# Optimization experiments

Measured on AMD Instinct MI355X. Metric: run time of the kernel, lower is better.

Reference implementation:

```python
import jax, jax.numpy as jnp
import numpy as np

N_NODES = 100000
N_EDGES = 3200000


def setup_inputs() -> dict:
    key = jax.random.key(0)
    k1, k2, k3, k4 = jax.random.split(key, 4)
    x = jax.random.normal(k1, (N_NODES, 3), dtype=jnp.float32)
    edge_index = jax.random.randint(k2, (2, N_EDGES), 0, N_NODES, dtype=jnp.int64)
    # Glorot-ish init for the two GCN layers
    W1 = jax.random.normal(k3, (3, 16), dtype=jnp.float32) * (1.0 / np.sqrt(3.0))
    b1 = jnp.zeros((16,), dtype=jnp.float32)
    W2 = jax.random.normal(k4, (16, 2), dtype=jnp.float32) * (1.0 / np.sqrt(16.0))
    b2 = jnp.zeros((2,), dtype=jnp.float32)
    return {"x": x, "edge_index": edge_index, "W1": W1, "b1": b1, "W2": W2, "b2": b2}


def gcn_conv(x, row, col, W, b, n_nodes):
    """PyG GCNConv: add self-loops, symmetric deg^-1/2 norm, linear, scatter-add, bias.
    row/col already include self-loops."""
    deg = jax.ops.segment_sum(jnp.ones_like(col, dtype=x.dtype), col, num_segments=n_nodes)
    dinv = jnp.where(deg > 0, deg ** -0.5, 0.0)
    norm = dinv[row] * dinv[col]            # [E+N]
    h = x @ W                               # [N, out]
    msg = h[row] * norm[:, None]            # gather + edge scale
    out = jax.ops.segment_sum(msg, col, num_segments=n_nodes)  # scatter-add to targets
    return out + b


def reference(x, edge_index, W1, b1, W2, b2):
    n = x.shape[0]
    loop = jnp.arange(n, dtype=edge_index.dtype)
    row = jnp.concatenate([edge_index[0], loop])
    col = jnp.concatenate([edge_index[1], loop])
    h = jax.nn.relu(gcn_conv(x, row, col, W1, b1, n))
    # dropout is identity in eval mode (training=False)
    h = gcn_conv(h, row, col, W2, b2, n)
    return jax.nn.log_softmax(h, axis=1)
```

## Files before the change

### kernel.cpp

```cpp
#include <hip/hip_runtime.h>
#include <math.h>

#define NN 100000
#define NB 32
#define NRANGE 8
#define RSZ 12500
#define CHUNK 1024
#define NCHUNK 98

#define W_FLAG  0
#define W_CNT   256
#define W_OFF   400256
#define W_DINV  800256
#define W_CSUM  1200256
#define W_CBASE 1201280
#define W_XS    1202304
#define W_HS2   2802304
#define W_B16   3602304
#define W_Z     10002304
#define SZ_RADIX 22802304
#define B_CNT   256
#define B_OFF   400256
#define B_CUR   800256
#define B_DINV  1200256
#define B_CSUM  1600256
#define B_CBASE 1601280
#define B_XS    1602560
#define B_HS2   3202560
#define B_RIDX  4002560
#define SZ_B    16802560

__global__ void k_detect(const void* ei, int* flag) {
    if (blockIdx.x == 0 && threadIdx.x == 0) {
        const long long* p = (const long long*)ei;
        int ok = 1;
        for (int i = 0; i < 64; ++i) {
            long long v = p[i];
            if (v < 0 || v >= NN) { ok = 0; break; }
        }
        *flag = ok;
    }
}

template <typename T>
__device__ __forceinline__ void phist_body(const T* __restrict__ col, long long E,
                                           unsigned* __restrict__ lcnt,
                                           unsigned short* __restrict__ cntP) {
    int r = blockIdx.x & (NRANGE - 1);
    int b = blockIdx.x >> 3;
    unsigned lo = (unsigned)r * RSZ;
    for (int i = threadIdx.x; i < RSZ; i += blockDim.x) lcnt[i] = 0u;
    __syncthreads();
    long long S = (E + NB - 1) / NB;
    long long sb = (long long)b * S;
    long long se = sb + S < E ? sb + S : E;
    long long B = blockDim.x;
    long long base = sb + threadIdx.x;
    long long nfull = (se - sb) / (4 * B);
    for (long long t = 0; t < nfull; ++t) {
        unsigned c0 = (unsigned)col[base];
        unsigned c1 = (unsigned)col[base + B];
        unsigned c2 = (unsigned)col[base + 2 * B];
        unsigned c3 = (unsigned)col[base + 3 * B];
        unsigned d0 = c0 - lo, d1 = c1 - lo, d2 = c2 - lo, d3 = c3 - lo;
        if (d0 < RSZ) atomicAdd(&lcnt[d0], 1u);
        if (d1 < RSZ) atomicAdd(&lcnt[d1], 1u);
        if (d2 < RSZ) atomicAdd(&lcnt[d2], 1u);
        if (d3 < RSZ) atomicAdd(&lcnt[d3], 1u);
        base += 4 * B;
    }
    for (long long e = base; e < se; e += B) {
        unsigned d = (unsigned)col[e] - lo;
        if (d < RSZ) atomicAdd(&lcnt[d], 1u);
    }
    __syncthreads();
    unsigned short* dst = cntP + (size_t)b * NN + lo;
    for (int i = threadIdx.x; i < RSZ; i += blockDim.x) dst[i] = (unsigned short)lcnt[i];
}
__global__ void k_phist(const void* ei, long long E, const int* flag,
                        unsigned short* cntP) {
    __shared__ unsigned lcnt[RSZ];
    if (*flag) phist_body(((const long long*)ei) + E, E, lcnt, cntP);
    else       phist_body(((const int*)ei) + E, E, lcnt, cntP);
}

__global__ void k_scanA(const unsigned short* __restrict__ cntP, unsigned* __restrict__ cnt,
                        unsigned* __restrict__ off, unsigned* __restrict__ csum) {
    __shared__ unsigned lds[256];
    int t = threadIdx.x;
    int base = blockIdx.x * CHUNK + t * 4;
    unsigned v[4] = {0u, 0u, 0u, 0u};
    if (base + 3 < NN) {
#pragma unroll
        for (int b = 0; b < NB; ++b) {
            const unsigned short* p = cntP + (size_t)b * NN + base;
            v[0] += p[0]; v[1] += p[1]; v[2] += p[2]; v[3] += p[3];
        }
    } else {
#pragma unroll
        for (int k = 0; k < 4; ++k) {
            int i = base + k;
            if (i < NN) { unsigned s = 0; for (int b = 0; b < NB; ++b) s += cntP[(size_t)b * NN + i]; v[k] = s; }
        }
    }
#pragma unroll
    for (int k = 0; k < 4; ++k) { int i = base + k; if (i < NN) cnt[i] = v[k]; }
    unsigned s = v[0] + v[1] + v[2] + v[3];
    lds[t] = s; __syncthreads();
    for (int o = 1; o < 256; o <<= 1) {
        unsigned add = (t >= o) ? lds[t - o] : 0u; __syncthreads();
        lds[t] += add; __syncthreads();
    }
    unsigned excl = lds[t] - s;
    if (t == 255) csum[blockIdx.x] = lds[255];
#pragma unroll
    for (int k = 0; k < 4; ++k) { int i = base + k; if (i < NN) off[i] = excl; excl += v[k]; }
}

__global__ void k_scan1(const unsigned* __restrict__ cnt, unsigned* __restrict__ off,
                        unsigned* __restrict__ csum) {
    __shared__ unsigned lds[256];
    int t = threadIdx.x;
    int base = blockIdx.x * CHUNK + t * 4;
    unsigned v[4];
#pragma unroll
    for (int k = 0; k < 4; ++k) { int i = base + k; v[k] = (i < NN) ? cnt[i] : 0u; }
    unsigned s = v[0] + v[1] + v[2] + v[3];
    lds[t] = s; __syncthreads();
    for (int o = 1; o < 256; o <<= 1) {
        unsigned add = (t >= o) ? lds[t - o] : 0u; __syncthreads();
        lds[t] += add; __syncthreads();
    }
    unsigned excl = lds[t] - s;
    if (t == 255) csum[blockIdx.x] = lds[255];
#pragma unroll
    for (int k = 0; k < 4; ++k) { int i = base + k; if (i < NN) off[i] = excl; excl += v[k]; }
}
__global__ void k_scan2(unsigned* __restrict__ csum, unsigned* __restrict__ cbase) {
    __shared__ unsigned lds[256];
    int t = threadIdx.x;
    unsigned s = (t < NCHUNK) ? csum[t] : 0u;
    lds[t] = s; __syncthreads();
    for (int o = 1; o < 256; o <<= 1) {
        unsigned add = (t >= o) ? lds[t - o] : 0u; __syncthreads();
        lds[t] += add; __syncthreads();
    }
    if (t < NCHUNK) cbase[t] = lds[t] - s;
}

__global__ void k_final(const unsigned short* __restrict__ cntP,
                        const unsigned* __restrict__ cbase, const unsigned* __restrict__ cnt,
                        unsigned* __restrict__ off, unsigned short* __restrict__ base16,
                        const float* __restrict__ x, float* __restrict__ dinv,
                        float4* __restrict__ xs) {
    int n = blockIdx.x * blockDim.x + threadIdx.x;
    if (n >= NN) return;
    unsigned o = off[n] + cbase[n >> 10];
    off[n] = o;
    unsigned run = 0;
#pragma unroll
    for (int b = 0; b < NB; ++b) {
        base16[(size_t)b * NN + n] = (unsigned short)run;
        run += cntP[(size_t)b * NN + n];
    }
    float d = rsqrtf((float)cnt[n] + 1.0f);
    dinv[n] = d;
    xs[n] = make_float4(x[3*n] * d, x[3*n+1] * d, x[3*n+2] * d, 0.f);
}

template <typename T>
__device__ __forceinline__ void pplace_body(const T* __restrict__ ei, long long E,
                                            const unsigned* __restrict__ off,
                                            const unsigned short* __restrict__ base16,
                                            unsigned* __restrict__ lcur,
                                            unsigned* __restrict__ ridx) {
    int r = blockIdx.x & (NRANGE - 1);
    int b = blockIdx.x >> 3;
    unsigned lo = (unsigned)r * RSZ;
    const unsigned short* bb = base16 + (size_t)b * NN + lo;
    const unsigned* oo = off + lo;
    for (int i = threadIdx.x; i < RSZ; i += blockDim.x) lcur[i] = oo[i] + bb[i];
    __syncthreads();
    const T* col = ei + E;
    long long S = (E + NB - 1) / NB;
    long long sb = (long long)b * S;
    long long se = sb + S < E ? sb + S : E;
    long long B = blockDim.x;
    long long base = sb + threadIdx.x;
    long long nfull = (se - sb) / (4 * B);
    for (long long t = 0; t < nfull; ++t) {
        long long e0 = base, e1 = base + B, e2 = base + 2 * B, e3 = base + 3 * B;
        unsigned d0 = (unsigned)col[e0] - lo;
        unsigned d1 = (unsigned)col[e1] - lo;
        unsigned d2 = (unsigned)col[e2] - lo;
        unsigned d3 = (unsigned)col[e3] - lo;
        if (d0 < RSZ) { unsigned p = atomicAdd(&lcur[d0], 1u); ridx[p] = (unsigned)ei[e0]; }
        if (d1 < RSZ) { unsigned p = atomicAdd(&lcur[d1], 1u); ridx[p] = (unsigned)ei[e1]; }
        if (d2 < RSZ) { unsigned p = atomicAdd(&lcur[d2], 1u); ridx[p] = (unsigned)ei[e2]; }
        if (d3 < RSZ) { unsigned p = atomicAdd(&lcur[d3], 1u); ridx[p] = (unsigned)ei[e3]; }
        base += 4 * B;
    }
    for (long long e = base; e < se; e += B) {
        unsigned d = (unsigned)col[e] - lo;
        if (d < RSZ) { unsigned p = atomicAdd(&lcur[d], 1u); ridx[p] = (unsigned)ei[e]; }
    }
}
__global__ void k_pplace(const void* ei, long long E, const int* flag,
                         const unsigned* off, const unsigned short* base16,
                         unsigned* ridx) {
    __shared__ unsigned lcur[RSZ];
    if (*flag) pplace_body((const long long*)ei, E, off, base16, lcur, ridx);
    else       pplace_body((const int*)ei, E, off, base16, lcur, ridx);
}

__global__ void k_lay1(const unsigned* __restrict__ off, const unsigned* __restrict__ cnt,
                       const unsigned* __restrict__ ridx, const float4* __restrict__ xs,
                       const float* __restrict__ dinv,
                       const float* __restrict__ W1, const float* __restrict__ b1,
                       const float* __restrict__ W2, float2* __restrict__ hs2) {
    int lane = threadIdx.x & 15;
    int node = blockIdx.x * (blockDim.x >> 4) + (threadIdx.x >> 4);
    if (node >= NN) return;
    unsigned s = off[node], n = cnt[node];
    float a0 = 0.f, a1 = 0.f, a2 = 0.f;
    for (unsigned k = lane; k < n; k += 16) {
        float4 v = xs[ridx[s + k]];
        a0 += v.x; a1 += v.y; a2 += v.z;
    }
#pragma unroll
    for (int m = 8; m; m >>= 1) {
        a0 += __shfl_xor(a0, m); a1 += __shfl_xor(a1, m); a2 += __shfl_xor(a2, m);
    }
    if (lane == 0) {
        float4 sv = xs[node];
        float d = dinv[node];
        float t0 = d*(a0+sv.x), t1 = d*(a1+sv.y), t2 = d*(a2+sv.z);
        float g0 = 0.f, g1 = 0.f;
#pragma unroll
        for (int j = 0; j < 16; ++j) {
            float h = fmaxf(fmaf(t0, W1[j], fmaf(t1, W1[16+j], fmaf(t2, W1[32+j], b1[j]))), 0.f);
            g0 = fmaf(h, W2[2*j],   g0);
            g1 = fmaf(h, W2[2*j+1], g1);
        }
        hs2[node] = make_float2(g0 * d, g1 * d);
    }
}
__global__ void k_lay2(const unsigned* __restrict__ off, const unsigned* __restrict__ cnt,
                       const unsigned* __restrict__ ridx, const float2* __restrict__ hs2,
                       const float* __restrict__ dinv, const float* __restrict__ b2,
                       float2* __restrict__ out) {
    int lane = threadIdx.x & 15;
    int node = blockIdx.x * (blockDim.x >> 4) + (threadIdx.x >> 4);
    if (node >= NN) return;
    unsigned s = off[node], n = cnt[node];
    float a0 = 0.f, a1 = 0.f;
    for (unsigned k = lane; k < n; k += 16) {
        float2 v = hs2[ridx[s + k]];
        a0 += v.x; a1 += v.y;
    }
#pragma unroll
    for (int m = 8; m; m >>= 1) {
        a0 += __shfl_xor(a0, m); a1 += __shfl_xor(a1, m);
    }
    if (lane == 0) {
        float2 sv = hs2[node];
        float d = dinv[node];
        float z0 = d*(a0+sv.x) + b2[0];
        float z1 = d*(a1+sv.y) + b2[1];
        float mx = fmaxf(z0, z1);
        float l  = mx + logf(expf(z0 - mx) + expf(z1 - mx));
        out[node] = make_float2(z0 - l, z1 - l);
    }
}

__global__ void k_zero(float4* z, long long n4) {
    long long stride = (long long)gridDim.x * blockDim.x;
    for (long long i = (long long)blockIdx.x * blockDim.x + threadIdx.x; i < n4; i += stride)
        z[i] = make_float4(0.f, 0.f, 0.f, 0.f);
}
template <typename T>
__device__ __forceinline__ void hist_loop(const T* __restrict__ col, long long E,
                                          unsigned* __restrict__ cnt) {
    long long stride = (long long)gridDim.x * blockDim.x;
    for (long long e = (long long)blockIdx.x * blockDim.x + threadIdx.x; e < E; e += stride)
        atomicAdd(&cnt[(unsigned)col[e]], 1u);
}
__global__ void k_histM(const void* ei, long long E, const int* flag, unsigned* cnt) {
    if (*flag) hist_loop(((const long long*)ei) + E, E, cnt);
    else       hist_loop(((const int*)ei) + E, E, cnt);
}
__global__ void k_scan3(const unsigned* __restrict__ cnt, const unsigned* __restrict__ cbase,
                        unsigned* __restrict__ off, unsigned* __restrict__ cur,
                        const float* __restrict__ x, float* __restrict__ dinv,
                        float4* __restrict__ xs) {
    int i = blockIdx.x * blockDim.x + threadIdx.x;
    if (i >= NN) return;
    unsigned o = off[i] + cbase[i >> 10];
    off[i] = o; cur[i] = o;
    float d = rsqrtf((float)cnt[i] + 1.0f);
    dinv[i] = d;
    xs[i] = make_float4(x[3*i] * d, x[3*i+1] * d, x[3*i+2] * d, 0.f);
}
template <typename T>
__device__ __forceinline__ void placeM_loop(const T* __restrict__ ei, long long E,
                                            unsigned* __restrict__ cur, unsigned* __restrict__ ridx) {
    long long stride = (long long)gridDim.x * blockDim.x;
    for (long long e = (long long)blockIdx.x * blockDim.x + threadIdx.x; e < E; e += stride) {
        unsigned c = (unsigned)ei[E + e];
        unsigned pos = atomicAdd(&cur[c], 1u);
        ridx[pos] = (unsigned)ei[e];
    }
}
__global__ void k_placeM(const void* ei, long long E, const int* flag,
                         unsigned* cur, unsigned* ridx) {
    if (*flag) placeM_loop((const long long*)ei, E, cur, ridx);
    else       placeM_loop((const int*)ei, E, cur, ridx);
}

extern "C" void kernel_launch(void* const* d_in, const int* in_sizes, int n_in,
                              void* d_out, int out_size, void* d_ws, size_t ws_size,
                              hipStream_t stream) {
    const float* x  = (const float*)d_in[0];
    const void*  ei = d_in[1];
    const float* W1 = (const float*)d_in[2];
    const float* b1 = (const float*)d_in[3];
    const float* W2 = (const float*)d_in[4];
    const float* b2 = (const float*)d_in[5];
    long long E = (long long)in_sizes[1] / 2;

    char* ws = (char*)d_ws;
    int* flag = (int*)(ws + W_FLAG);
    float2* out = (float2*)d_out;

    int ngrid = (NN + 255) / 256;
    int lgrid = (NN + 15) / 16;

    k_detect<<<1, 64, 0, stream>>>(ei, flag);

    if (ws_size >= SZ_RADIX) {
        unsigned*       cnt    = (unsigned*)(ws + W_CNT);
        unsigned*       off    = (unsigned*)(ws + W_OFF);
        float*          dinv   = (float*)(ws + W_DINV);
        unsigned*       csum   = (unsigned*)(ws + W_CSUM);
        unsigned*       cbase  = (unsigned*)(ws + W_CBASE);
        float4*         xs     = (float4*)(ws + W_XS);
        float2*         hs2    = (float2*)(ws + W_HS2);
        unsigned short* base16 = (unsigned short*)(ws + W_B16);
        unsigned short* cntP   = (unsigned short*)(ws + W_Z);
        unsigned*       ridx   = (unsigned*)(ws + W_Z);

        k_phist <<<NRANGE * NB, 1024, 0, stream>>>(ei, E, flag, cntP);
        k_scanA <<<NCHUNK, 256, 0, stream>>>(cntP, cnt, off, csum);
        k_scan2 <<<1, 256, 0, stream>>>(csum, cbase);
        k_final <<<ngrid, 256, 0, stream>>>(cntP, cbase, cnt, off, base16, x, dinv, xs);
        k_pplace<<<NRANGE * NB, 1024, 0, stream>>>(ei, E, flag, off, base16, ridx);
        k_lay1  <<<lgrid, 256, 0, stream>>>(off, cnt, ridx, xs, dinv, W1, b1, W2, hs2);
        k_lay2  <<<lgrid, 256, 0, stream>>>(off, cnt, ridx, hs2, dinv, b2, out);
    } else if (ws_size >= SZ_B) {
        unsigned* cnt   = (unsigned*)(ws + B_CNT);
        unsigned* off   = (unsigned*)(ws + B_OFF);
        unsigned* cur   = (unsigned*)(ws + B_CUR);
        float*    dinv  = (float*)(ws + B_DINV);
        unsigned* csum  = (unsigned*)(ws + B_CSUM);
        unsigned* cbase = (unsigned*)(ws + B_CBASE);
        float4*   xs    = (float4*)(ws + B_XS);
        float2*   hs2   = (float2*)(ws + B_HS2);
        unsigned* ridx  = (unsigned*)(ws + B_RIDX);
        long long eg = (E + 255) / 256;
        int egrid = (int)(eg > 4096 ? 4096 : eg);

        k_zero  <<<98, 256, 0, stream>>>((float4*)(ws + B_CNT), 25000);
        k_histM <<<egrid, 256, 0, stream>>>(ei, E, flag, cnt);
        k_scan1 <<<NCHUNK, 256, 0, stream>>>(cnt, off, csum);
        k_scan2 <<<1, 256, 0, stream>>>(csum, cbase);
        k_scan3 <<<ngrid, 256, 0, stream>>>(cnt, cbase, off, cur, x, dinv, xs);
        k_placeM<<<egrid, 256, 0, stream>>>(ei, E, flag, cur, ridx);
        k_lay1  <<<lgrid, 256, 0, stream>>>(off, cnt, ridx, xs, dinv, W1, b1, W2, hs2);
        k_lay2  <<<lgrid, 256, 0, stream>>>(off, cnt, ridx, hs2, dinv, b2, out);
    }
}
```

Measured before the change: 208.7 us.

## Add two-pass bucketed staging of edges before per-range histogram and placement

Result: faster. 176.4 us (-15.5%).

```diff
diff --git a/kernel.cpp b/kernel.cpp
--- a/kernel.cpp
+++ b/kernel.cpp
@@ -5,9 +5,26 @@
 #define NB 32
 #define NRANGE 8
 #define RSZ 12500
+#define NS 256
 #define CHUNK 1024
 #define NCHUNK 98
 
+#define S_FLAG  0
+#define S_BCNT  256
+#define S_BOFF  8448
+#define S_ROFF  16640
+#define S_CNT   16896
+#define S_OFF   416896
+#define S_DINV  816896
+#define S_CSUM  1216896
+#define S_CBASE 1217536
+#define S_XS    1218048
+#define S_HS2   2818048
+#define S_B16   3618048
+#define S_STG   10018048
+#define S_CNTP  22818048
+#define S_RIDX  22818048
+#define SZ_S    35618048
 #define W_FLAG  0
 #define W_CNT   256
 #define W_OFF   400256
@@ -43,45 +60,148 @@
 }
 
 template <typename T>
-__device__ __forceinline__ void phist_body(const T* __restrict__ col, long long E,
-                                           unsigned* __restrict__ lcnt,
-                                           unsigned short* __restrict__ cntP) {
-    int r = blockIdx.x & (NRANGE - 1);
-    int b = blockIdx.x >> 3;
-    unsigned lo = (unsigned)r * RSZ;
-    for (int i = threadIdx.x; i < RSZ; i += blockDim.x) lcnt[i] = 0u;
-    __syncthreads();
-    long long S = (E + NB - 1) / NB;
-    long long sb = (long long)b * S;
-    long long se = sb + S < E ? sb + S : E;
+__device__ __forceinline__ void bcount_body(const T* __restrict__ col, long long E,
+                                            unsigned* __restrict__ lds8,
+                                            unsigned* __restrict__ bucketCnt) {
+    int s = blockIdx.x;
+    for (int i = threadIdx.x; i < 8 * 64; i += blockDim.x) lds8[i] = 0u;
+    __syncthreads();
+    long long S = (E + NS - 1) / NS;
+    long long sb = (long long)s * S, se = sb + S < E ? sb + S : E;
     long long B = blockDim.x;
     long long base = sb + threadIdx.x;
+    int lane = threadIdx.x & 63;
     long long nfull = (se - sb) / (4 * B);
     for (long long t = 0; t < nfull; ++t) {
         unsigned c0 = (unsigned)col[base];
         unsigned c1 = (unsigned)col[base + B];
         unsigned c2 = (unsigned)col[base + 2 * B];
         unsigned c3 = (unsigned)col[base + 3 * B];
-        unsigned d0 = c0 - lo, d1 = c1 - lo, d2 = c2 - lo, d3 = c3 - lo;
-        if (d0 < RSZ) atomicAdd(&lcnt[d0], 1u);
-        if (d1 < RSZ) atomicAdd(&lcnt[d1], 1u);
-        if (d2 < RSZ) atomicAdd(&lcnt[d2], 1u);
-        if (d3 < RSZ) atomicAdd(&lcnt[d3], 1u);
+        atomicAdd(&lds8[(c0 / RSZ) * 64 + lane], 1u);
+        atomicAdd(&lds8[(c1 / RSZ) * 64 + lane], 1u);
+        atomicAdd(&lds8[(c2 / RSZ) * 64 + lane], 1u);
+        atomicAdd(&lds8[(c3 / RSZ) * 64 + lane], 1u);
         base += 4 * B;
     }
+    for (long long e = base; e < se; e += B)
+        atomicAdd(&lds8[((unsigned)col[e] / RSZ) * 64 + lane], 1u);
+    __syncthreads();
+    if (threadIdx.x < 8) {
+        unsigned t = 0;
+        for (int j = 0; j < 64; ++j) t += lds8[threadIdx.x * 64 + j];
+        bucketCnt[s * 8 + threadIdx.x] = t;
+    }
+}
+__global__ void k_bcount(const void* ei, long long E, const int* flag,
+                         unsigned* bucketCnt) {
+    __shared__ unsigned lds8[8 * 64];
+    if (*flag) bcount_body(((const long long*)ei) + E, E, lds8, bucketCnt);
+    else       bcount_body(((const int*)ei) + E, E, lds8, bucketCnt);
+}
+
+__global__ void k_bscan(const unsigned* __restrict__ bucketCnt,
+                        unsigned* __restrict__ bucketOff, unsigned* __restrict__ rangeOff) {
+    __shared__ unsigned lds[1024];
+    int t = threadIdx.x;
+    int j0 = 2 * t, j1 = 2 * t + 1;
+    unsigned v0 = bucketCnt[(j0 & (NS - 1)) * 8 + (j0 >> 8)];
+    unsigned v1 = bucketCnt[(j1 & (NS - 1)) * 8 + (j1 >> 8)];
+    unsigned s = v0 + v1;
+    lds[t] = s; __syncthreads();
+    for (int o = 1; o < 1024; o <<= 1) {
+        unsigned add = (t >= o) ? lds[t - o] : 0u; __syncthreads();
+        lds[t] += add; __syncthreads();
+    }
+    unsigned excl = lds[t] - s;
+    bucketOff[j0] = excl;
+    bucketOff[j1] = excl + v0;
+    if ((j0 & (NS - 1)) == 0) rangeOff[j0 >> 8] = excl;
+    if (t == 1023) rangeOff[8] = lds[1023];
+}
+
+template <typename T>
+__device__ __forceinline__ void stage_body(const T* __restrict__ ei, long long E,
+                                           const unsigned* __restrict__ bucketOff,
+                                           unsigned* __restrict__ lcur,
+                                           unsigned* __restrict__ staged) {
+    int s = blockIdx.x;
+    if (threadIdx.x < 8) lcur[threadIdx.x] = bucketOff[threadIdx.x * NS + s];
+    __syncthreads();
+    const T* col = ei + E;
+    long long S = (E + NS - 1) / NS;
+    long long sb = (long long)s * S, se = sb + S < E ? sb + S : E;
+    long long B = blockDim.x;
+    long long base = sb + threadIdx.x;
+    long long nfull = (se - sb) / (4 * B);
+    for (long long t = 0; t < nfull; ++t) {
+        long long e0 = base, e1 = base + B, e2 = base + 2 * B, e3 = base + 3 * B;
+        unsigned c0 = (unsigned)col[e0], c1 = (unsigned)col[e1];
+        unsigned c2 = (unsigned)col[e2], c3 = (unsigned)col[e3];
+        unsigned r0 = (unsigned)ei[e0], r1 = (unsigned)ei[e1];
+        unsigned r2 = (unsigned)ei[e2], r3 = (unsigned)ei[e3];
+        unsigned g0 = c0 / RSZ, g1 = c1 / RSZ, g2 = c2 / RSZ, g3 = c3 / RSZ;
+        unsigned p0 = atomicAdd(&lcur[g0], 1u);
+        unsigned p1 = atomicAdd(&lcur[g1], 1u);
+        unsigned p2 = atomicAdd(&lcur[g2], 1u);
+        unsigned p3 = atomicAdd(&lcur[g3], 1u);
+        staged[p0] = (r0 << 14) | (c0 - g0 * RSZ);
+        staged[p1] = (r1 << 14) | (c1 - g1 * RSZ);
+        staged[p2] = (r2 << 14) | (c2 - g2 * RSZ);
+        staged[p3] = (r3 << 14) | (c3 - g3 * RSZ);
+        base += 4 * B;
+    }
     for (long long e = base; e < se; e += B) {
-        unsigned d = (unsigned)col[e] - lo;
-        if (d < RSZ) atomicAdd(&lcnt[d], 1u);
-    }
-    __syncthreads();
-    unsigned short* dst = cntP + (size_t)b * NN + lo;
+        unsigned c = (unsigned)col[e], r = (unsigned)ei[e];
+        unsigned g = c / RSZ;
+        unsigned p = atomicAdd(&lcur[g], 1u);
+        staged[p] = (r << 14) | (c - g * RSZ);
+    }
+}
+__global__ void k_stage(const void* ei, long long E, const int* flag,
+                        const unsigned* bucketOff, unsigned* staged) {
+    __shared__ unsigned lcur[8];
+    if (*flag) stage_body((const long long*)ei, E, bucketOff, lcur, staged);
+    else       stage_body((const int*)ei, E, bucketOff, lcur, staged);
+}
+
+__global__ void k_shist(const unsigned* __restrict__ staged, const unsigned* __restrict__ rangeOff,
+                        unsigned short* __restrict__ cntP) {
+    __shared__ unsigned lcnt[RSZ];
+    int r = blockIdx.x & (NRANGE - 1);
+    int s = blockIdx.x >> 3;
+    for (int i = threadIdx.x; i < RSZ; i += blockDim.x) lcnt[i] = 0u;
+    __syncthreads();
+    unsigned A = rangeOff[r], Bnd = rangeOff[r + 1];
+    unsigned L = (Bnd - A + NB - 1) / NB;
+    unsigned cb = A + s * L;
+    unsigned ce = cb + L < Bnd ? cb + L : Bnd;
+    for (unsigned i = cb + threadIdx.x; i < ce; i += blockDim.x)
+        atomicAdd(&lcnt[staged[i] & 16383u], 1u);
+    __syncthreads();
+    unsigned short* dst = cntP + (size_t)s * NN + (unsigned)r * RSZ;
     for (int i = threadIdx.x; i < RSZ; i += blockDim.x) dst[i] = (unsigned short)lcnt[i];
 }
-__global__ void k_phist(const void* ei, long long E, const int* flag,
-                        unsigned short* cntP) {
-    __shared__ unsigned lcnt[RSZ];
-    if (*flag) phist_body(((const long long*)ei) + E, E, lcnt, cntP);
-    else       phist_body(((const int*)ei) + E, E, lcnt, cntP);
+
+__global__ void k_splace(const unsigned* __restrict__ staged, const unsigned* __restrict__ rangeOff,
+                         const unsigned* __restrict__ off, const unsigned short* __restrict__ base16,
+                         unsigned* __restrict__ ridx) {
+    __shared__ unsigned lcur[RSZ];
+    int r = blockIdx.x & (NRANGE - 1);
+    int s = blockIdx.x >> 3;
+    unsigned lo = (unsigned)r * RSZ;
+    const unsigned short* bb = base16 + (size_t)s * NN + lo;
+    const unsigned* oo = off + lo;
+    for (int i = threadIdx.x; i < RSZ; i += blockDim.x) lcur[i] = oo[i] + bb[i];
+    __syncthreads();
+    unsigned A = rangeOff[r], Bnd = rangeOff[r + 1];
+    unsigned L = (Bnd - A + NB - 1) / NB;
+    unsigned cb = A + s * L;
+    unsigned ce = cb + L < Bnd ? cb + L : Bnd;
+    for (unsigned i = cb + threadIdx.x; i < ce; i += blockDim.x) {
+        unsigned p = staged[i];
+        unsigned pos = atomicAdd(&lcur[p & 16383u], 1u);
+        ridx[pos] = p >> 14;
+    }
 }
 
 __global__ void k_scanA(const unsigned short* __restrict__ cntP, unsigned* __restrict__ cnt,
@@ -116,7 +236,6 @@
 #pragma unroll
     for (int k = 0; k < 4; ++k) { int i = base + k; if (i < NN) off[i] = excl; excl += v[k]; }
 }
-
 __global__ void k_scan1(const unsigned* __restrict__ cnt, unsigned* __restrict__ off,
                         unsigned* __restrict__ csum) {
     __shared__ unsigned lds[256];
@@ -147,7 +266,6 @@
     }
     if (t < NCHUNK) cbase[t] = lds[t] - s;
 }
-
 __global__ void k_final(const unsigned short* __restrict__ cntP,
                         const unsigned* __restrict__ cbase, const unsigned* __restrict__ cnt,
                         unsigned* __restrict__ off, unsigned short* __restrict__ base16,
@@ -167,7 +285,105 @@
     dinv[n] = d;
     xs[n] = make_float4(x[3*n] * d, x[3*n+1] * d, x[3*n+2] * d, 0.f);
 }
-
+__global__ void k_lay1(const unsigned* __restrict__ off, const unsigned* __restrict__ cnt,
+                       const unsigned* __restrict__ ridx, const float4* __restrict__ xs,
+                       const float* __restrict__ dinv,
+                       const float* __restrict__ W1, const float* __restrict__ b1,
+                       const float* __restrict__ W2, float2* __restrict__ hs2) {
+    int lane = threadIdx.x & 15;
+    int node = blockIdx.x * (blockDim.x >> 4) + (threadIdx.x >> 4);
+    if (node >= NN) return;
+    unsigned s = off[node], n = cnt[node];
+    float a0 = 0.f, a1 = 0.f, a2 = 0.f;
+    for (unsigned k = lane; k < n; k += 16) {
+        float4 v = xs[ridx[s + k]];
+        a0 += v.x; a1 += v.y; a2 += v.z;
+    }
+#pragma unroll
+    for (int m = 8; m; m >>= 1) {
+        a0 += __shfl_xor(a0, m); a1 += __shfl_xor(a1, m); a2 += __shfl_xor(a2, m);
+    }
+    if (lane == 0) {
+        float4 sv = xs[node];
+        float d = dinv[node];
+        float t0 = d*(a0+sv.x), t1 = d*(a1+sv.y), t2 = d*(a2+sv.z);
+        float g0 = 0.f, g1 = 0.f;
+#pragma unroll
+        for (int j = 0; j < 16; ++j) {
+            float h = fmaxf(fmaf(t0, W1[j], fmaf(t1, W1[16+j], fmaf(t2, W1[32+j], b1[j]))), 0.f);
+            g0 = fmaf(h, W2[2*j],   g0);
+            g1 = fmaf(h, W2[2*j+1], g1);
+        }
+        hs2[node] = make_float2(g0 * d, g1 * d);
+    }
+}
+__global__ void k_lay2(const unsigned* __restrict__ off, const unsigned* __restrict__ cnt,
+                       const unsigned* __restrict__ ridx, const float2* __restrict__ hs2,
+                       const float* __restrict__ dinv, const float* __restrict__ b2,
+                       float2* __restrict__ out) {
+    int lane = threadIdx.x & 15;
+    int node = blockIdx.x * (blockDim.x >> 4) + (threadIdx.x >> 4);
+    if (node >= NN) return;
+    unsigned s = off[node], n = cnt[node];
+    float a0 = 0.f, a1 = 0.f;
+    for (unsigned k = lane; k < n; k += 16) {
+        float2 v = hs2[ridx[s + k]];
+        a0 += v.x; a1 += v.y;
+    }
+#pragma unroll
+    for (int m = 8; m; m >>= 1) {
+        a0 += __shfl_xor(a0, m); a1 += __shfl_xor(a1, m);
+    }
+    if (lane == 0) {
+        float2 sv = hs2[node];
+        float d = dinv[node];
+        float z0 = d*(a0+sv.x) + b2[0];
+        float z1 = d*(a1+sv.y) + b2[1];
+        float mx = fmaxf(z0, z1);
+        float l  = mx + logf(expf(z0 - mx) + expf(z1 - mx));
+        out[node] = make_float2(z0 - l, z1 - l);
+    }
+}
+
+template <typename T>
+__device__ __forceinline__ void phist_body(const T* __restrict__ col, long long E,
+                                           unsigned* __restrict__ lcnt,
+                                           unsigned short* __restrict__ cntP) {
+    int r = blockIdx.x & (NRANGE - 1);
+    int b = blockIdx.x >> 3;
+    unsigned lo = (unsigned)r * RSZ;
+    for (int i = threadIdx.x; i < RSZ; i += blockDim.x) lcnt[i] = 0u;
+    __syncthreads();
+    long long S = (E + NB - 1) / NB;
+    long long sb = (long long)b * S, se = sb + S < E ? sb + S : E;
+    long long B = blockDim.x;
+    long long base = sb + threadIdx.x;
+    long long nfull = (se - sb) / (4 * B);
+    for (long long t = 0; t < nfull; ++t) {
+        unsigned d0 = (unsigned)col[base] - lo;
+        unsigned d1 = (unsigned)col[base + B] - lo;
+        unsigned d2 = (unsigned)col[base + 2 * B] - lo;
+        unsigned d3 = (unsigned)col[base + 3 * B] - lo;
+        if (d0 < RSZ) atomicAdd(&lcnt[d0], 1u);
+        if (d1 < RSZ) atomicAdd(&lcnt[d1], 1u);
+        if (d2 < RSZ) atomicAdd(&lcnt[d2], 1u);
+        if (d3 < RSZ) atomicAdd(&lcnt[d3], 1u);
+        base += 4 * B;
+    }
+    for (long long e = base; e < se; e += B) {
+        unsigned d = (unsigned)col[e] - lo;
+        if (d < RSZ) atomicAdd(&lcnt[d], 1u);
+    }
+    __syncthreads();
+    unsigned short* dst = cntP + (size_t)b * NN + lo;
+    for (int i = threadIdx.x; i < RSZ; i += blockDim.x) dst[i] = (unsigned short)lcnt[i];
+}
+__global__ void k_phist(const void* ei, long long E, const int* flag,
+                        unsigned short* cntP) {
+    __shared__ unsigned lcnt[RSZ];
+    if (*flag) phist_body(((const long long*)ei) + E, E, lcnt, cntP);
+    else       phist_body(((const int*)ei) + E, E, lcnt, cntP);
+}
 template <typename T>
 __device__ __forceinline__ void pplace_body(const T* __restrict__ ei, long long E,
                                             const unsigned* __restrict__ off,
@@ -183,8 +399,7 @@
     __syncthreads();
     const T* col = ei + E;
     long long S = (E + NB - 1) / NB;
-    long long sb = (long long)b * S;
-    long long se = sb + S < E ? sb + S : E;
+    long long sb = (long long)b * S, se = sb + S < E ? sb + S : E;
     long long B = blockDim.x;
     long long base = sb + threadIdx.x;
     long long nfull = (se - sb) / (4 * B);
@@ -213,66 +428,6 @@
     else       pplace_body((const int*)ei, E, off, base16, lcur, ridx);
 }
 
-__global__ void k_lay1(const unsigned* __restrict__ off, const unsigned* __restrict__ cnt,
-                       const unsigned* __restrict__ ridx, const float4* __restrict__ xs,
-                       const float* __restrict__ dinv,
-                       const float* __restrict__ W1, const float* __restrict__ b1,
-                       const float* __restrict__ W2, float2* __restrict__ hs2) {
-    int lane = threadIdx.x & 15;
-    int node = blockIdx.x * (blockDim.x >> 4) + (threadIdx.x >> 4);
-    if (node >= NN) return;
-    unsigned s = off[node], n = cnt[node];
-    float a0 = 0.f, a1 = 0.f, a2 = 0.f;
-    for (unsigned k = lane; k < n; k += 16) {
-        float4 v = xs[ridx[s + k]];
-        a0 += v.x; a1 += v.y; a2 += v.z;
-    }
-#pragma unroll
-    for (int m = 8; m; m >>= 1) {
-        a0 += __shfl_xor(a0, m); a1 += __shfl_xor(a1, m); a2 += __shfl_xor(a2, m);
-    }
-    if (lane == 0) {
-        float4 sv = xs[node];
-        float d = dinv[node];
-        float t0 = d*(a0+sv.x), t1 = d*(a1+sv.y), t2 = d*(a2+sv.z);
-        float g0 = 0.f, g1 = 0.f;
-#pragma unroll
-        for (int j = 0; j < 16; ++j) {
-            float h = fmaxf(fmaf(t0, W1[j], fmaf(t1, W1[16+j], fmaf(t2, W1[32+j], b1[j]))), 0.f);
-            g0 = fmaf(h, W2[2*j],   g0);
-            g1 = fmaf(h, W2[2*j+1], g1);
-        }
-        hs2[node] = make_float2(g0 * d, g1 * d);
-    }
-}
-__global__ void k_lay2(const unsigned* __restrict__ off, const unsigned* __restrict__ cnt,
-                       const unsigned* __restrict__ ridx, const float2* __restrict__ hs2,
-                       const float* __restrict__ dinv, const float* __restrict__ b2,
-                       float2* __restrict__ out) {
-    int lane = threadIdx.x & 15;
-    int node = blockIdx.x * (blockDim.x >> 4) + (threadIdx.x >> 4);
-    if (node >= NN) return;
-    unsigned s = off[node], n = cnt[node];
-    float a0 = 0.f, a1 = 0.f;
-    for (unsigned k = lane; k < n; k += 16) {
-        float2 v = hs2[ridx[s + k]];
-        a0 += v.x; a1 += v.y;
-    }
-#pragma unroll
-    for (int m = 8; m; m >>= 1) {
-        a0 += __shfl_xor(a0, m); a1 += __shfl_xor(a1, m);
-    }
-    if (lane == 0) {
-        float2 sv = hs2[node];
-        float d = dinv[node];
-        float z0 = d*(a0+sv.x) + b2[0];
-        float z1 = d*(a1+sv.y) + b2[1];
-        float mx = fmaxf(z0, z1);
-        float l  = mx + logf(expf(z0 - mx) + expf(z1 - mx));
-        out[node] = make_float2(z0 - l, z1 - l);
-    }
-}
-
 __global__ void k_zero(float4* z, long long n4) {
     long long stride = (long long)gridDim.x * blockDim.x;
     for (long long i = (long long)blockIdx.x * blockDim.x + threadIdx.x; i < n4; i += stride)
@@ -329,15 +484,41 @@
     long long E = (long long)in_sizes[1] / 2;
 
     char* ws = (char*)d_ws;
-    int* flag = (int*)(ws + W_FLAG);
     float2* out = (float2*)d_out;
-
     int ngrid = (NN + 255) / 256;
     int lgrid = (NN + 15) / 16;
 
-    k_detect<<<1, 64, 0, stream>>>(ei, flag);
-
-    if (ws_size >= SZ_RADIX) {
+    k_detect<<<1, 64, 0, stream>>>(ei, (int*)ws);
+
+    if (ws_size >= SZ_S) {
+        int*            flag   = (int*)(ws + S_FLAG);
+        unsigned*       bcnt   = (unsigned*)(ws + S_BCNT);
+        unsigned*       boff   = (unsigned*)(ws + S_BOFF);
+        unsigned*       roff   = (unsigned*)(ws + S_ROFF);
+        unsigned*       cnt    = (unsigned*)(ws + S_CNT);
+        unsigned*       off    = (unsigned*)(ws + S_OFF);
+        float*          dinv   = (float*)(ws + S_DINV);
+        unsigned*       csum   = (unsigned*)(ws + S_CSUM);
+        unsigned*       cbase  = (unsigned*)(ws + S_CBASE);
+        float4*         xs     = (float4*)(ws + S_XS);
+        float2*         hs2    = (float2*)(ws + S_HS2);
+        unsigned short* base16 = (unsigned short*)(ws + S_B16);
+        unsigned*       staged = (unsigned*)(ws + S_STG);
+        unsigned short* cntP   = (unsigned short*)(ws + S_CNTP);
+        unsigned*       ridx   = (unsigned*)(ws + S_RIDX);
+
+        k_bcount<<<NS, 1024, 0, stream>>>(ei, E, flag, bcnt);
+        k_bscan <<<1, 1024, 0, stream>>>(bcnt, boff, roff);
+        k_stage <<<NS, 1024, 0, stream>>>(ei, E, flag, boff, staged);
+        k_shist <<<NRANGE * NB, 1024, 0, stream>>>(staged, roff, cntP);
+        k_scanA <<<NCHUNK, 256, 0, stream>>>(cntP, cnt, off, csum);
+        k_scan2 <<<1, 256, 0, stream>>>(csum, cbase);
+        k_final <<<ngrid, 256, 0, stream>>>(cntP, cbase, cnt, off, base16, x, dinv, xs);
+        k_splace<<<NRANGE * NB, 1024, 0, stream>>>(staged, roff, off, base16, ridx);
+        k_lay1  <<<lgrid, 256, 0, stream>>>(off, cnt, ridx, xs, dinv, W1, b1, W2, hs2);
+        k_lay2  <<<lgrid, 256, 0, stream>>>(off, cnt, ridx, hs2, dinv, b2, out);
+    } else if (ws_size >= SZ_RADIX) {
+        int*            flag   = (int*)(ws + W_FLAG);
         unsigned*       cnt    = (unsigned*)(ws + W_CNT);
         unsigned*       off    = (unsigned*)(ws + W_OFF);
         float*          dinv   = (float*)(ws + W_DINV);
@@ -357,6 +538,7 @@
         k_lay1  <<<lgrid, 256, 0, stream>>>(off, cnt, ridx, xs, dinv, W1, b1, W2, hs2);
         k_lay2  <<<lgrid, 256, 0, stream>>>(off, cnt, ridx, hs2, dinv, b2, out);
     } else if (ws_size >= SZ_B) {
+        int*      flag  = (int*)(ws + B_CNT - 256);
         unsigned* cnt   = (unsigned*)(ws + B_CNT);
         unsigned* off   = (unsigned*)(ws + B_OFF);
         unsigned* cur   = (unsigned*)(ws + B_CUR);
```
